# Kernel tuning notes

Hardware: AMD Instinct MI355X
Metric: run time of the kernel (lower is better)

The kernel has to match this reference:

```python
import jax, jax.numpy as jnp
import numpy as np

N = 50000
E = 800000
DIN = 128
# SAGEConv layer dims: (in, out). conv0: input->embed; hidden: 128->64->128->256->512
DIMS = [(128, 128), (128, 64), (64, 128), (128, 256), (256, 512)]
NUM_CLASSES = 4


def setup_inputs() -> dict:
    key = jax.random.key(0)
    ks = jax.random.split(key, 3 * len(DIMS) + 4)
    inp = {"x": jax.random.normal(ks[0], (N, DIN), dtype=jnp.float32)}
    for i, (din, dout) in enumerate(DIMS):
        s = 1.0 / np.sqrt(din).astype(np.float32)
        inp[f"Wl{i}"] = jax.random.normal(ks[1 + 3 * i], (dout, din), dtype=jnp.float32) * s
        inp[f"bl{i}"] = jnp.zeros((dout,), dtype=jnp.float32)
        inp[f"Wr{i}"] = jax.random.normal(ks[2 + 3 * i], (dout, din), dtype=jnp.float32) * s
    dlast = DIMS[-1][1]
    inp["Wout"] = jax.random.normal(ks[-2], (NUM_CLASSES, dlast), dtype=jnp.float32) * (1.0 / np.sqrt(dlast).astype(np.float32))
    inp["bout"] = jnp.zeros((NUM_CLASSES,), dtype=jnp.float32)
    inp["edge_index"] = jax.random.randint(ks[-1], (2, E), 0, N, dtype=jnp.int32)
    return inp


def _forward(x, params, edge_index):
    src, dst = edge_index[0], edge_index[1]
    n = x.shape[0]
    # in-degree (count of incoming edges), clamped to >= 1 as in PyG mean aggregation
    deg = jax.ops.segment_sum(jnp.ones((src.shape[0],), x.dtype), dst, num_segments=n)
    deg_inv = (1.0 / jnp.maximum(deg, 1.0))[:, None]

    def sage(h, Wl, bl, Wr):
        # mean aggregation over incoming neighbors, then lin_l(agg) + lin_r(h)
        agg = jax.ops.segment_sum(h[src], dst, num_segments=n) * deg_inv
        return agg @ Wl.T + bl + h @ Wr.T

    h = x
    for i in range(len(DIMS)):
        h = jax.nn.relu(sage(h, params[f"Wl{i}"], params[f"bl{i}"], params[f"Wr{i}"]))
    logits = h @ params["Wout"].T + params["bout"]
    return jax.nn.softmax(logits, axis=-1)


def reference(x, Wl0, bl0, Wr0, Wl1, bl1, Wr1, Wl2, bl2, Wr2, Wl3, bl3, Wr3,
              Wl4, bl4, Wr4, Wout, bout, edge_index):
    params = {"Wl0": Wl0, "bl0": bl0, "Wr0": Wr0, "Wl1": Wl1, "bl1": bl1, "Wr1": Wr1,
              "Wl2": Wl2, "bl2": bl2, "Wr2": Wr2, "Wl3": Wl3, "bl3": bl3, "Wr3": Wr3,
              "Wl4": Wl4, "bl4": bl4, "Wr4": Wr4, "Wout": Wout, "bout": bout}
    return _forward(x, params, edge_index)
```

## Files before the change

### kernel.cpp

```cpp
#include <hip/hip_runtime.h>
#include <hip/hip_bf16.h>
#include <cstdint>
#include <cstddef>


typedef short bf16x8 __attribute__((ext_vector_type(8)));
typedef float f32x16 __attribute__((ext_vector_type(16)));

static inline int idiv_up(int a, int b) { return (a + b - 1) / b; }

static __device__ __forceinline__ float bf2f(unsigned short u) {
  union { unsigned int i; float f; } v; v.i = ((unsigned int)u) << 16; return v.f;
}
static __device__ __forceinline__ unsigned short f2bf(float f) {
  union { float f; unsigned int i; } v; v.f = f;
  return (unsigned short)((v.i + 0x7FFFu + ((v.i >> 16) & 1u)) >> 16);
}
static __device__ __forceinline__ float lo16(unsigned int u) { return bf2f((unsigned short)(u & 0xffffu)); }
static __device__ __forceinline__ float hi16(unsigned int u) { return bf2f((unsigned short)(u >> 16)); }
static __device__ __forceinline__ unsigned int packbf(float a, float b) {
  return (unsigned int)f2bf(a) | ((unsigned int)f2bf(b) << 16);
}

static __device__ __forceinline__ void gl_lds16(const void* g, void* l) {
  typedef __attribute__((address_space(3))) unsigned int lds_u32;
  typedef __attribute__((address_space(1))) const unsigned int glb_u32;
  __builtin_amdgcn_global_load_lds((glb_u32*)(uintptr_t)g,
                                   (lds_u32*)(unsigned int)(uintptr_t)l, 16, 0, 0);
}

__global__ void k_count_deg(const int* __restrict__ dst, int* __restrict__ deg, int E) {
  const int T = gridDim.x * blockDim.x;
  const int e0 = blockIdx.x * blockDim.x + threadIdx.x;
#pragma unroll
  for (int j = 0; j < 4; ++j) {
    const int e = e0 + j * T;
    if (e < E) atomicAdd(deg + dst[e], 1);
  }
}

__global__ __launch_bounds__(1024)
void k_scan1(const int* __restrict__ deg, int* __restrict__ loc, int* __restrict__ part, int n) {
  __shared__ int wsum[16];
  const int tid = threadIdx.x;
  const int lane = tid & 63, wid = tid >> 6;
  const int i = blockIdx.x * 1024 + tid;
  const int v = (i < n) ? deg[i] : 0;
  int incl = v;
#pragma unroll
  for (int off = 1; off < 64; off <<= 1) {
    int t = __shfl_up(incl, off);
    if (lane >= off) incl += t;
  }
  if (lane == 63) wsum[wid] = incl;
  __syncthreads();
  if (wid == 0) {
    int wv = (lane < 16) ? wsum[lane] : 0;
#pragma unroll
    for (int off = 1; off < 16; off <<= 1) {
      int t = __shfl_up(wv, off);
      if (lane >= off) wv += t;
    }
    if (lane < 16) wsum[lane] = wv;
  }
  __syncthreads();
  const int woff = (wid > 0) ? wsum[wid - 1] : 0;
  if (i < n) loc[i] = woff + incl;
  if (tid == 1023) part[blockIdx.x] = woff + incl;
}

__global__ __launch_bounds__(1024)
void k_scan2(int* __restrict__ part, int nb) {
  __shared__ int wsum[16];
  const int tid = threadIdx.x;
  const int lane = tid & 63, wid = tid >> 6;
  const int v = (tid < nb) ? part[tid] : 0;
  int incl = v;
#pragma unroll
  for (int off = 1; off < 64; off <<= 1) {
    int t = __shfl_up(incl, off);
    if (lane >= off) incl += t;
  }
  if (lane == 63) wsum[wid] = incl;
  __syncthreads();
  if (wid == 0) {
    int wv = (lane < 16) ? wsum[lane] : 0;
#pragma unroll
    for (int off = 1; off < 16; off <<= 1) {
      int t = __shfl_up(wv, off);
      if (lane >= off) wv += t;
    }
    if (lane < 16) wsum[lane] = wv;
  }
  __syncthreads();
  const int woff = (wid > 0) ? wsum[wid - 1] : 0;
  if (tid < nb) part[tid] = woff + incl - v;
  if (tid == 0) part[nb] = wsum[15];
}

__global__ __launch_bounds__(256)
void k_scan3(const int* __restrict__ deg, const int* __restrict__ loc, const int* __restrict__ part,
             int* __restrict__ row_off, int* __restrict__ cursor, float* __restrict__ deg_inv,
             int n, int nb) {
  const int i = blockIdx.x * blockDim.x + threadIdx.x;
  if (i < n) {
    const int v = deg[i];
    const int ro = part[i >> 10] + loc[i] - v;
    row_off[i] = ro;
    cursor[i] = ro;
    deg_inv[i] = 1.0f / (float)((v > 1) ? v : 1);
  }
  if (i == 0) row_off[n] = part[nb];
}

__global__ void k_fill_csr(const int* __restrict__ src, const int* __restrict__ dst,
                           int* __restrict__ cursor, int* __restrict__ esrc, int E) {
  const int T = gridDim.x * blockDim.x;
  const int e0 = blockIdx.x * blockDim.x + threadIdx.x;
  int dv[4], sv[4], pv[4];
#pragma unroll
  for (int j = 0; j < 4; ++j) {
    const int e = e0 + j * T;
    if (e < E) { dv[j] = dst[e]; sv[j] = src[e]; }
  }
#pragma unroll
  for (int j = 0; j < 4; ++j) {
    const int e = e0 + j * T;
    if (e < E) pv[j] = atomicAdd(cursor + dv[j], 1);
  }
#pragma unroll
  for (int j = 0; j < 4; ++j) {
    const int e = e0 + j * T;
    if (e < E) esrc[pv[j]] = sv[j];
  }
}

__global__ __launch_bounds__(256)
void k_conv_x(const float* __restrict__ src, unsigned short* __restrict__ dst, int n4) {
  for (int i = blockIdx.x * blockDim.x + threadIdx.x; i < n4; i += gridDim.x * blockDim.x) {
    const float4 v = *((const float4*)src + i);
    uint2 o;
    o.x = packbf(v.x, v.y);
    o.y = packbf(v.z, v.w);
    *((uint2*)dst + i) = o;
  }
}

struct PackJob { const float* src; unsigned short* dst; int O; int K; int colOff; int Opack; };
struct PackJobs { PackJob j[10]; };

__global__ __launch_bounds__(256)
void k_pack_w(PackJobs jobs) {
  const PackJob J = jobs.j[blockIdx.y];
  const int total = J.O * J.K / 2;
  for (int u = blockIdx.x * blockDim.x + threadIdx.x; u < total; u += gridDim.x * blockDim.x) {
    const int e = u * 2;
    const int col = e / J.K;
    const int k = e - col * J.K;
    const int kt = k >> 6, ch = (k >> 3) & 7, j = k & 7;
    const float f0 = J.src[(size_t)col * J.K + k];
    const float f1 = J.src[(size_t)col * J.K + k + 1];
    const int didx = kt * (J.Opack * 64) + ch * (J.Opack * 8) + (col + J.colOff) * 8 + j;
    ((unsigned int*)J.dst)[didx >> 1] = packbf(f0, f1);
  }
}

static __device__ __forceinline__ void acc_u4(float* acc, const uint4& v) {
  acc[0] += lo16(v.x); acc[1] += hi16(v.x);
  acc[2] += lo16(v.y); acc[3] += hi16(v.y);
  acc[4] += lo16(v.z); acc[5] += hi16(v.z);
  acc[6] += lo16(v.w); acc[7] += hi16(v.w);
}

__global__ __launch_bounds__(256)
void k_agg128(const unsigned short* __restrict__ h, const int* __restrict__ row_off,
              const int* __restrict__ esrc, const float* __restrict__ deg_inv,
              unsigned short* __restrict__ agg, int N) {
  const int node = blockIdx.x * 4 + (threadIdx.x >> 6);
  if (node >= N) return;
  const int lane = threadIdx.x & 63;
  const int g = lane >> 4, c = lane & 15;
  const int s0 = row_off[node], s1 = row_off[node + 1];
  const uint4* hp = (const uint4*)h;
  float acc[8] = {0.f, 0.f, 0.f, 0.f, 0.f, 0.f, 0.f, 0.f};
  for (int i = s0; i < s1; i += 32) {
    int el = i + (lane & 31);
    if (el >= s1) el = s1 - 1;
    const int ev = esrc[el];
    uint4 v[8];
#pragma unroll
    for (int u = 0; u < 8; ++u) {
      if (i + u * 4 < s1) {
        const int e = __shfl(ev, u * 4 + g);
        v[u] = hp[(size_t)e * 16 + c];
      }
    }
#pragma unroll
    for (int u = 0; u < 8; ++u)
      if (i + u * 4 + g < s1) acc_u4(acc, v[u]);
  }
#pragma unroll
  for (int j = 0; j < 8; ++j) {
    acc[j] += __shfl_xor(acc[j], 16);
    acc[j] += __shfl_xor(acc[j], 32);
  }
  if (g == 0) {
    const float di = deg_inv[node];
    uint4 o;
    o.x = packbf(acc[0] * di, acc[1] * di);
    o.y = packbf(acc[2] * di, acc[3] * di);
    o.z = packbf(acc[4] * di, acc[5] * di);
    o.w = packbf(acc[6] * di, acc[7] * di);
    ((uint4*)agg)[(size_t)node * 16 + c] = o;
  }
}

__global__ __launch_bounds__(256)
void k_agg256(const unsigned short* __restrict__ h, const int* __restrict__ row_off,
              const int* __restrict__ esrc, const float* __restrict__ deg_inv,
              unsigned short* __restrict__ agg, int N) {
  const int node = blockIdx.x * 4 + (threadIdx.x >> 6);
  if (node >= N) return;
  const int lane = threadIdx.x & 63;
  const int g = lane >> 5, c = lane & 31;
  const int s0 = row_off[node], s1 = row_off[node + 1];
  const uint4* hp = (const uint4*)h;
  float acc[8] = {0.f, 0.f, 0.f, 0.f, 0.f, 0.f, 0.f, 0.f};
  for (int i = s0; i < s1; i += 32) {
    int el = i + (lane & 31);
    if (el >= s1) el = s1 - 1;
    const int ev = esrc[el];
    uint4 v[16];
#pragma unroll
    for (int u = 0; u < 16; ++u) {
      if (i + u * 2 < s1) {
        const int e = __shfl(ev, u * 2 + g);
        v[u] = hp[(size_t)e * 32 + c];
      }
    }
#pragma unroll
    for (int u = 0; u < 16; ++u)
      if (i + u * 2 + g < s1) acc_u4(acc, v[u]);
  }
#pragma unroll
  for (int j = 0; j < 8; ++j) acc[j] += __shfl_xor(acc[j], 32);
  if (g == 0) {
    const float di = deg_inv[node];
    uint4 o;
    o.x = packbf(acc[0] * di, acc[1] * di);
    o.y = packbf(acc[2] * di, acc[3] * di);
    o.z = packbf(acc[4] * di, acc[5] * di);
    o.w = packbf(acc[6] * di, acc[7] * di);
    ((uint4*)agg)[(size_t)node * 32 + c] = o;
  }
}

__global__ __launch_bounds__(256)
void k_agg64(const unsigned short* __restrict__ h, const int* __restrict__ row_off,
             const int* __restrict__ esrc, const float* __restrict__ deg_inv,
             unsigned short* __restrict__ agg, int N) {
  const int node = blockIdx.x * 4 + (threadIdx.x >> 6);
  if (node >= N) return;
  const int lane = threadIdx.x & 63;
  const int g = lane >> 3, c = lane & 7;
  const int s0 = row_off[node], s1 = row_off[node + 1];
  const uint4* hp = (const uint4*)h;
  float acc[8] = {0.f, 0.f, 0.f, 0.f, 0.f, 0.f, 0.f, 0.f};
  for (int i = s0; i < s1; i += 32) {
    int el = i + (lane & 31);
    if (el >= s1) el = s1 - 1;
    const int ev = esrc[el];
    uint4 v[4];
#pragma unroll
    for (int u = 0; u < 4; ++u) {
      if (i + u * 8 < s1) {
        const int e = __shfl(ev, u * 8 + g);
        v[u] = hp[(size_t)e * 8 + c];
      }
    }
#pragma unroll
    for (int u = 0; u < 4; ++u)
      if (i + u * 8 + g < s1) acc_u4(acc, v[u]);
  }
#pragma unroll
  for (int j = 0; j < 8; ++j) {
    acc[j] += __shfl_xor(acc[j], 8);
    acc[j] += __shfl_xor(acc[j], 16);
    acc[j] += __shfl_xor(acc[j], 32);
  }
  if (g == 0) {
    const float di = deg_inv[node];
    uint4 o;
    o.x = packbf(acc[0] * di, acc[1] * di);
    o.y = packbf(acc[2] * di, acc[3] * di);
    o.z = packbf(acc[4] * di, acc[5] * di);
    o.w = packbf(acc[6] * di, acc[7] * di);
    ((uint4*)agg)[(size_t)node * 8 + c] = o;
  }
}

__global__ __launch_bounds__(256)
void k_agg_post64(const unsigned short* __restrict__ z, const int* __restrict__ row_off,
                  const int* __restrict__ esrc, const float* __restrict__ deg_inv,
                  const float* __restrict__ bias, unsigned short* __restrict__ out, int N) {
  const int node = blockIdx.x * 4 + (threadIdx.x >> 6);
  if (node >= N) return;
  const int lane = threadIdx.x & 63;
  const int g = lane >> 3, c = lane & 7;
  const int s0 = row_off[node], s1 = row_off[node + 1];
  const uint4* zp = (const uint4*)z;
  float acc[8] = {0.f, 0.f, 0.f, 0.f, 0.f, 0.f, 0.f, 0.f};
  for (int i = s0; i < s1; i += 32) {
    int el = i + (lane & 31);
    if (el >= s1) el = s1 - 1;
    const int ev = esrc[el];
    uint4 v[4];
#pragma unroll
    for (int u = 0; u < 4; ++u) {
      if (i + u * 8 < s1) {
        const int e = __shfl(ev, u * 8 + g);
        v[u] = zp[(size_t)e * 16 + c];
      }
    }
#pragma unroll
    for (int u = 0; u < 4; ++u)
      if (i + u * 8 + g < s1) acc_u4(acc, v[u]);
  }
#pragma unroll
  for (int j = 0; j < 8; ++j) {
    acc[j] += __shfl_xor(acc[j], 8);
    acc[j] += __shfl_xor(acc[j], 16);
    acc[j] += __shfl_xor(acc[j], 32);
  }
  if (g == 0) {
    const float di = deg_inv[node];
    const uint4 yr = zp[(size_t)node * 16 + 8 + c];
    float y[8];
    y[0] = lo16(yr.x); y[1] = hi16(yr.x); y[2] = lo16(yr.y); y[3] = hi16(yr.y);
    y[4] = lo16(yr.z); y[5] = hi16(yr.z); y[6] = lo16(yr.w); y[7] = hi16(yr.w);
    float r[8];
#pragma unroll
    for (int j = 0; j < 8; ++j)
      r[j] = fmaxf(acc[j] * di + y[j] + bias[c * 8 + j], 0.f);
    uint4 o;
    o.x = packbf(r[0], r[1]);
    o.y = packbf(r[2], r[3]);
    o.z = packbf(r[4], r[5]);
    o.w = packbf(r[6], r[7]);
    ((uint4*)out)[(size_t)node * 8 + c] = o;
  }
}

template <int WC, int NCB, bool FUSED>
__global__ __launch_bounds__(WC * 128)
void k_sage_gemm(const unsigned short* __restrict__ A0, const unsigned short* __restrict__ B0,
                 const unsigned short* __restrict__ A1, const unsigned short* __restrict__ B1,
                 const float* __restrict__ bias, unsigned short* __restrict__ C,
                 int Nn, int K, int O) {
  constexpr int BN = WC * 64;
  constexpr int T = WC * 128;
  constexpr int ACH = 1024;
  constexpr int LPT = ACH / T;
  __shared__ char lds[2 * 16384];

  const int nrp = (Nn + 127) >> 7;
  const int bid = blockIdx.x;
  const int r8 = bid & 7;
  const int tb = bid >> 3;
  const int cb = tb % NCB;
  const int rowp = (tb / NCB) * 8 + r8;
  if (rowp >= nrp) return;

  const int tid = threadIdx.x;
  const int w = tid >> 6, lane = tid & 63;
  const int wr = w / WC, wc = w % WC;
  const int fr = lane & 31, fq = lane >> 5;
  const int row0 = rowp * 128 + wr * 64;
  const int colb = cb * BN;

  const int KT0 = K >> 6;
  const int NT = FUSED ? 2 * KT0 : KT0;

  f32x16 acc[2][2];
#pragma unroll
  for (int m = 0; m < 2; ++m)
#pragma unroll
    for (int cn = 0; cn < 2; ++cn)
#pragma unroll
      for (int r = 0; r < 16; ++r) acc[m][cn][r] = 0.f;

  auto stage = [&](int buf, int t) {
    const unsigned short* Ab;
    int ktl;
    if (FUSED) {
      const int ph = (t >= KT0) ? 1 : 0;
      Ab = ph ? A1 : A0;
      ktl = t - ph * KT0;
    } else {
      Ab = A0; ktl = t;
    }
    char* lb = lds + buf * 16384;
#pragma unroll
    for (int i = 0; i < LPT; ++i) {
      const int ch = tid + i * T;
      const int ar = ch >> 3, s = ch & 7;
      int g = rowp * 128 + ar;
      if (g >= Nn) g = Nn - 1;
      gl_lds16(Ab + (size_t)g * K + ktl * 64 + ((s ^ (ar & 7)) << 3), lb + ch * 16);
    }
  };

  stage(0, 0);
#pragma unroll 1
  for (int t = 0; t < NT; ++t) {
    asm volatile("s_waitcnt vmcnt(0)" ::: "memory");
    __syncthreads();
    const unsigned short* Bp;
    int ktl;
    if (FUSED) {
      const int ph = (t >= KT0) ? 1 : 0;
      Bp = ph ? B1 : B0;
      ktl = t - ph * KT0;
    } else {
      Bp = B0; ktl = t;
    }
    const unsigned short* Bbase = Bp + (size_t)ktl * (O * 64) + (size_t)(colb + wc * 64) * 8;
    bf16x8 bg[4][2];
#pragma unroll
    for (int k16i = 0; k16i < 4; ++k16i) {
      const int c = k16i * 2 + fq;
#pragma unroll
      for (int cn = 0; cn < 2; ++cn)
        bg[k16i][cn] = *(const bf16x8*)(Bbase + (size_t)c * (O * 8) + (cn * 32 + fr) * 8);
    }
    if (t + 1 < NT) stage((t + 1) & 1, t + 1);
    const char* lb = lds + (t & 1) * 16384;
#pragma unroll
    for (int k16i = 0; k16i < 4; ++k16i) {
      const int c = k16i * 2 + fq;
      bf16x8 af[2];
#pragma unroll
      for (int m = 0; m < 2; ++m) {
        const int rl = wr * 64 + m * 32 + fr;
        af[m] = *(const bf16x8*)(lb + rl * 128 + ((c ^ (rl & 7)) << 4));
      }
#pragma unroll
      for (int m = 0; m < 2; ++m)
#pragma unroll
        for (int cn = 0; cn < 2; ++cn)
          acc[m][cn] = __builtin_amdgcn_mfma_f32_32x32x16_bf16(af[m], bg[k16i][cn], acc[m][cn], 0, 0, 0);
    }
  }

#pragma unroll
  for (int cn = 0; cn < 2; ++cn) {
    const int col = colb + wc * 64 + cn * 32 + fr;
    float bb = 0.f;
    if (FUSED) bb = bias[col];
#pragma unroll
    for (int m = 0; m < 2; ++m) {
#pragma unroll
      for (int reg = 0; reg < 16; ++reg) {
        float v = acc[m][cn][reg];
        if (FUSED) v = fmaxf(v + bb, 0.f);
        const float nb = __shfl_xor(v, 1);
        const int row = row0 + m * 32 + (reg & 3) + 8 * (reg >> 2) + 4 * fq;
        if (!(lane & 1) && row < Nn) {
          *(unsigned int*)(C + (size_t)row * O + col) = packbf(v, nb);
        }
      }
    }
  }
}

__global__ __launch_bounds__(256)
void k_out_softmax(const unsigned short* __restrict__ h, const float* __restrict__ W4,
                   const float* __restrict__ b, float* __restrict__ out, int N) {
  __shared__ float w[2048];
  const int tid = threadIdx.x;
#pragma unroll
  for (int i = 0; i < 8; ++i) w[tid + i * 256] = W4[tid + i * 256];
  __syncthreads();
  const int n = blockIdx.x * 4 + (tid >> 6);
  if (n >= N) return;
  const int lane = tid & 63;
  const unsigned int* hp = (const unsigned int*)h + (size_t)n * 256;
  float a[4] = {0.f, 0.f, 0.f, 0.f};
#pragma unroll
  for (int it = 0; it < 4; ++it) {
    const unsigned int v = hp[it * 64 + lane];
    const float lo = lo16(v);
    const float hi = hi16(v);
    const int k = (it * 64 + lane) * 2;
#pragma unroll
    for (int c = 0; c < 4; ++c)
      a[c] += lo * w[c * 512 + k] + hi * w[c * 512 + k + 1];
  }
#pragma unroll
  for (int off = 32; off > 0; off >>= 1) {
#pragma unroll
    for (int c = 0; c < 4; ++c) a[c] += __shfl_down(a[c], off);
  }
  if (lane == 0) {
    const float l0 = a[0] + b[0], l1 = a[1] + b[1], l2 = a[2] + b[2], l3 = a[3] + b[3];
    const float m = fmaxf(fmaxf(l0, l1), fmaxf(l2, l3));
    const float e0 = expf(l0 - m), e1 = expf(l1 - m), e2 = expf(l2 - m), e3 = expf(l3 - m);
    const float inv = 1.0f / (e0 + e1 + e2 + e3);
    float4 r; r.x = e0 * inv; r.y = e1 * inv; r.z = e2 * inv; r.w = e3 * inv;
    *(float4*)(out + (size_t)n * 4) = r;
  }
}

extern "C" void kernel_launch(void* const* d_in, const int* in_sizes, int n_in,
                              void* d_out, int out_size, void* d_ws, size_t ws_size,
                              hipStream_t stream) {
  const float* x = (const float*)d_in[0];
  const float* Wl[5] = {(const float*)d_in[1], (const float*)d_in[4], (const float*)d_in[7],
                        (const float*)d_in[10], (const float*)d_in[13]};
  const float* bl[5] = {(const float*)d_in[2], (const float*)d_in[5], (const float*)d_in[8],
                        (const float*)d_in[11], (const float*)d_in[14]};
  const float* Wr[5] = {(const float*)d_in[3], (const float*)d_in[6], (const float*)d_in[9],
                        (const float*)d_in[12], (const float*)d_in[15]};
  const float* Wout = (const float*)d_in[16];
  const float* bout = (const float*)d_in[17];
  const int* eidx = (const int*)d_in[18];

  const int N = in_sizes[0] / 128;
  const int E = in_sizes[18] / 2;
  const int* srcI = eidx;
  const int* dstI = eidx + E;

  const int Kd[5] = {128, 128, 64, 128, 256};
  const int Od[5] = {128, 64, 128, 256, 512};

  char* ws = (char*)d_ws;
  size_t p = 0;
  auto alloc = [&](size_t bytes) { size_t r = p; p += (bytes + 255) & ~(size_t)255; return r; };
  int*   deg     = (int*)(ws + alloc((size_t)N * 4));
  int*   row_off = (int*)(ws + alloc((size_t)(N + 1) * 4));
  int*   cursor  = (int*)(ws + alloc((size_t)N * 4));
  float* deg_inv = (float*)(ws + alloc((size_t)N * 4));
  int*   loc     = (int*)(ws + alloc((size_t)N * 4));
  int*   part    = (int*)(ws + alloc((size_t)1032 * 4));
  int*   esrc    = (int*)(ws + alloc((size_t)E * 4));
  unsigned short* xb = (unsigned short*)(ws + alloc((size_t)N * 128 * 2));
  unsigned short* wlb[5];
  unsigned short* wrb[5];
  for (int l = 0; l < 5; ++l) {
    wlb[l] = (unsigned short*)(ws + alloc((size_t)Od[l] * Kd[l] * 2));
    wrb[l] = (unsigned short*)(ws + alloc((size_t)Od[l] * Kd[l] * 2));
  }
  unsigned short* wcat1 = (unsigned short*)(ws + alloc((size_t)128 * 128 * 2));
  unsigned short* bufA = (unsigned short*)(ws + alloc((size_t)N * 512 * 2));
  unsigned short* bufB = (unsigned short*)(ws + alloc((size_t)N * 256 * 2));
  unsigned short* agg  = (unsigned short*)(ws + alloc((size_t)N * 256 * 2));
  (void)ws_size; (void)n_in; (void)out_size;

  k_conv_x<<<128, 256, 0, stream>>>(x, xb, N * 128 / 4);
  PackJobs jobs;
  for (int l = 0; l < 5; ++l) {
    if (l == 1) {
      jobs.j[2] = {Wl[1], wcat1, 64, 128, 0, 128};
      jobs.j[3] = {Wr[1], wcat1, 64, 128, 64, 128};
    } else {
      jobs.j[2 * l]     = {Wl[l], wlb[l], Od[l], Kd[l], 0, Od[l]};
      jobs.j[2 * l + 1] = {Wr[l], wrb[l], Od[l], Kd[l], 0, Od[l]};
    }
  }
  k_pack_w<<<dim3(32, 10), 256, 0, stream>>>(jobs);

  hipMemsetAsync(deg, 0, (size_t)N * 4, stream);
  k_count_deg<<<idiv_up(E, 1024), 256, 0, stream>>>(dstI, deg, E);
  const int nb = idiv_up(N, 1024);
  k_scan1<<<nb, 1024, 0, stream>>>(deg, loc, part, N);
  k_scan2<<<1, 1024, 0, stream>>>(part, nb);
  k_scan3<<<idiv_up(N + 1, 256), 256, 0, stream>>>(deg, loc, part, row_off, cursor, deg_inv, N, nb);
  k_fill_csr<<<idiv_up(E, 1024), 256, 0, stream>>>(srcI, dstI, cursor, esrc, E);

  const int gx8 = 8 * ((idiv_up(N, 128) + 7) / 8);

  k_agg128<<<idiv_up(N, 4), 256, 0, stream>>>(xb, row_off, esrc, deg_inv, agg, N);
  k_sage_gemm<2, 1, true><<<gx8, 256, 0, stream>>>(agg, wlb[0], xb, wrb[0], bl[0], bufA, N, 128, 128);

  k_sage_gemm<2, 1, false><<<gx8, 256, 0, stream>>>(bufA, wcat1, bufA, wcat1, bl[1], agg, N, 128, 128);
  k_agg_post64<<<idiv_up(N, 4), 256, 0, stream>>>(agg, row_off, esrc, deg_inv, bl[1], bufB, N);

  k_agg64<<<idiv_up(N, 4), 256, 0, stream>>>(bufB, row_off, esrc, deg_inv, agg, N);
  k_sage_gemm<2, 1, true><<<gx8, 256, 0, stream>>>(agg, wlb[2], bufB, wrb[2], bl[2], bufA, N, 64, 128);

  k_agg128<<<idiv_up(N, 4), 256, 0, stream>>>(bufA, row_off, esrc, deg_inv, agg, N);
  k_sage_gemm<2, 2, true><<<2 * gx8, 256, 0, stream>>>(agg, wlb[3], bufA, wrb[3], bl[3], bufB, N, 128, 256);

  k_agg256<<<idiv_up(N, 4), 256, 0, stream>>>(bufB, row_off, esrc, deg_inv, agg, N);
  k_sage_gemm<2, 4, true><<<4 * gx8, 256, 0, stream>>>(agg, wlb[4], bufB, wrb[4], bl[4], bufA, N, 256, 512);

  k_out_softmax<<<idiv_up(N, 4), 256, 0, stream>>>(bufA, Wout, bout, (float*)d_out, N);
}
```

Baseline: 393.8 us.

## Fuse output head projection into last SAGE GEMM epilogue and widen CSR build loops

The last SAGE GEMM no longer writes the N×512 bf16 hidden activation to global memory. Each block stages its ReLU'd tile in LDS and computes partial 4-class logits against its 128-column slice of Wout, writing per-column-block partials. A small final kernel sums the four partials, adds the bias and applies softmax. This avoids writing and re-reading about 51 MB of activations, at the cost of an extra LDS pass and two syncs per block. The degree-count and CSR-fill kernels also now process 8 edges per thread with half the grid.

```diff
diff --git a/kernel.cpp b/kernel.cpp
--- a/kernel.cpp
+++ b/kernel.cpp
@@ -33,7 +33,7 @@
   const int T = gridDim.x * blockDim.x;
   const int e0 = blockIdx.x * blockDim.x + threadIdx.x;
 #pragma unroll
-  for (int j = 0; j < 4; ++j) {
+  for (int j = 0; j < 8; ++j) {
     const int e = e0 + j * T;
     if (e < E) atomicAdd(deg + dst[e], 1);
   }
@@ -117,19 +117,19 @@
                            int* __restrict__ cursor, int* __restrict__ esrc, int E) {
   const int T = gridDim.x * blockDim.x;
   const int e0 = blockIdx.x * blockDim.x + threadIdx.x;
-  int dv[4], sv[4], pv[4];
-#pragma unroll
-  for (int j = 0; j < 4; ++j) {
+  int dv[8], sv[8], pv[8];
+#pragma unroll
+  for (int j = 0; j < 8; ++j) {
     const int e = e0 + j * T;
     if (e < E) { dv[j] = dst[e]; sv[j] = src[e]; }
   }
 #pragma unroll
-  for (int j = 0; j < 4; ++j) {
+  for (int j = 0; j < 8; ++j) {
     const int e = e0 + j * T;
     if (e < E) pv[j] = atomicAdd(cursor + dv[j], 1);
   }
 #pragma unroll
-  for (int j = 0; j < 4; ++j) {
+  for (int j = 0; j < 8; ++j) {
     const int e = e0 + j * T;
     if (e < E) esrc[pv[j]] = sv[j];
   }
@@ -351,17 +351,19 @@
   }
 }
 
-template <int WC, int NCB, bool FUSED>
+template <int WC, int NCB, bool FUSED, bool HEAD>
 __global__ __launch_bounds__(WC * 128)
 void k_sage_gemm(const unsigned short* __restrict__ A0, const unsigned short* __restrict__ B0,
                  const unsigned short* __restrict__ A1, const unsigned short* __restrict__ B1,
                  const float* __restrict__ bias, unsigned short* __restrict__ C,
+                 const float* __restrict__ W4g, float* __restrict__ Pb,
                  int Nn, int K, int O) {
   constexpr int BN = WC * 64;
   constexpr int T = WC * 128;
   constexpr int ACH = 1024;
   constexpr int LPT = ACH / T;
-  __shared__ char lds[2 * 16384];
+  constexpr int LDS_SZ = HEAD ? (2 * 16384 + 2048) : (2 * 16384);
+  __shared__ char lds[LDS_SZ];
 
   const int nrp = (Nn + 127) >> 7;
   const int bid = blockIdx.x;
@@ -377,6 +379,21 @@
   const int fr = lane & 31, fq = lane >> 5;
   const int row0 = rowp * 128 + wr * 64;
   const int colb = cb * BN;
+
+  if constexpr (HEAD) {
+    float* w4s = (float*)(lds + 32768);
+#pragma unroll
+    for (int ii = 0; ii < 2 * BN * 4 / T / 2; ++ii) {
+      const int idx = tid * 2 + ii;
+    }
+    const int i0 = tid * 2;
+#pragma unroll
+    for (int ii = 0; ii < 2; ++ii) {
+      const int idx = i0 + ii;
+      if (idx < 4 * BN)
+        w4s[idx] = W4g[(idx >> 7) * 512 + colb + (idx & (BN - 1))];
+    }
+  }
 
   const int KT0 = K >> 6;
   const int NT = FUSED ? 2 * KT0 : KT0;
@@ -452,6 +469,51 @@
     }
   }
 
+  if constexpr (HEAD) {
+    __syncthreads();
+    unsigned int* lh = (unsigned int*)lds;
+    float* w4s = (float*)(lds + 32768);
+#pragma unroll
+    for (int cn = 0; cn < 2; ++cn) {
+      const int coll = wc * 64 + cn * 32 + fr;
+      const float bb = bias[colb + coll];
+#pragma unroll
+      for (int m = 0; m < 2; ++m) {
+#pragma unroll
+        for (int reg = 0; reg < 16; ++reg) {
+          const float v = fmaxf(acc[m][cn][reg] + bb, 0.f);
+          const float nb = __shfl_xor(v, 1);
+          const int rowl = wr * 64 + m * 32 + (reg & 3) + 8 * (reg >> 2) + 4 * fq;
+          if (!(lane & 1)) {
+            const int c2 = coll >> 1;
+            lh[rowl * 64 + ((c2 + rowl) & 63)] = packbf(v, nb);
+          }
+        }
+      }
+    }
+    __syncthreads();
+    if (tid < 128) {
+      const int rowl = tid;
+      float p0 = 0.f, p1 = 0.f, p2 = 0.f, p3 = 0.f;
+#pragma unroll
+      for (int j = 0; j < 64; ++j) {
+        const unsigned int u = lh[rowl * 64 + ((j + rowl) & 63)];
+        const float lo = lo16(u), hi = hi16(u);
+        const int cl = 2 * j, ch = 2 * j + 1;
+        p0 += lo * w4s[cl] + hi * w4s[ch];
+        p1 += lo * w4s[128 + cl] + hi * w4s[128 + ch];
+        p2 += lo * w4s[256 + cl] + hi * w4s[256 + ch];
+        p3 += lo * w4s[384 + cl] + hi * w4s[384 + ch];
+      }
+      const int rg = rowp * 128 + rowl;
+      if (rg < Nn) {
+        float4 o; o.x = p0; o.y = p1; o.z = p2; o.w = p3;
+        *(float4*)(Pb + ((size_t)cb * Nn + rg) * 4) = o;
+      }
+    }
+    return;
+  }
+
 #pragma unroll
   for (int cn = 0; cn < 2; ++cn) {
     const int col = colb + wc * 64 + cn * 32 + fr;
@@ -474,41 +536,23 @@
 }
 
 __global__ __launch_bounds__(256)
-void k_out_softmax(const unsigned short* __restrict__ h, const float* __restrict__ W4,
-                   const float* __restrict__ b, float* __restrict__ out, int N) {
-  __shared__ float w[2048];
-  const int tid = threadIdx.x;
-#pragma unroll
-  for (int i = 0; i < 8; ++i) w[tid + i * 256] = W4[tid + i * 256];
-  __syncthreads();
-  const int n = blockIdx.x * 4 + (tid >> 6);
+void k_head_final(const float* __restrict__ Pb, const float* __restrict__ b,
+                  float* __restrict__ out, int N) {
+  const int n = blockIdx.x * blockDim.x + threadIdx.x;
   if (n >= N) return;
-  const int lane = tid & 63;
-  const unsigned int* hp = (const unsigned int*)h + (size_t)n * 256;
-  float a[4] = {0.f, 0.f, 0.f, 0.f};
-#pragma unroll
-  for (int it = 0; it < 4; ++it) {
-    const unsigned int v = hp[it * 64 + lane];
-    const float lo = lo16(v);
-    const float hi = hi16(v);
-    const int k = (it * 64 + lane) * 2;
-#pragma unroll
-    for (int c = 0; c < 4; ++c)
-      a[c] += lo * w[c * 512 + k] + hi * w[c * 512 + k + 1];
-  }
-#pragma unroll
-  for (int off = 32; off > 0; off >>= 1) {
-#pragma unroll
-    for (int c = 0; c < 4; ++c) a[c] += __shfl_down(a[c], off);
-  }
-  if (lane == 0) {
-    const float l0 = a[0] + b[0], l1 = a[1] + b[1], l2 = a[2] + b[2], l3 = a[3] + b[3];
-    const float m = fmaxf(fmaxf(l0, l1), fmaxf(l2, l3));
-    const float e0 = expf(l0 - m), e1 = expf(l1 - m), e2 = expf(l2 - m), e3 = expf(l3 - m);
-    const float inv = 1.0f / (e0 + e1 + e2 + e3);
-    float4 r; r.x = e0 * inv; r.y = e1 * inv; r.z = e2 * inv; r.w = e3 * inv;
-    *(float4*)(out + (size_t)n * 4) = r;
-  }
+  const float4 q0 = *(const float4*)(Pb + (size_t)n * 4);
+  const float4 q1 = *(const float4*)(Pb + ((size_t)N + n) * 4);
+  const float4 q2 = *(const float4*)(Pb + ((size_t)2 * N + n) * 4);
+  const float4 q3 = *(const float4*)(Pb + ((size_t)3 * N + n) * 4);
+  const float l0 = q0.x + q1.x + q2.x + q3.x + b[0];
+  const float l1 = q0.y + q1.y + q2.y + q3.y + b[1];
+  const float l2 = q0.z + q1.z + q2.z + q3.z + b[2];
+  const float l3 = q0.w + q1.w + q2.w + q3.w + b[3];
+  const float m = fmaxf(fmaxf(l0, l1), fmaxf(l2, l3));
+  const float e0 = expf(l0 - m), e1 = expf(l1 - m), e2 = expf(l2 - m), e3 = expf(l3 - m);
+  const float inv = 1.0f / (e0 + e1 + e2 + e3);
+  float4 r; r.x = e0 * inv; r.y = e1 * inv; r.z = e2 * inv; r.w = e3 * inv;
+  *(float4*)(out + (size_t)n * 4) = r;
 }
 
 extern "C" void kernel_launch(void* const* d_in, const int* in_sizes, int n_in,
@@ -554,6 +598,7 @@
   unsigned short* bufA = (unsigned short*)(ws + alloc((size_t)N * 512 * 2));
   unsigned short* bufB = (unsigned short*)(ws + alloc((size_t)N * 256 * 2));
   unsigned short* agg  = (unsigned short*)(ws + alloc((size_t)N * 256 * 2));
+  float* Pb = (float*)(ws + alloc((size_t)4 * N * 4 * 4));
   (void)ws_size; (void)n_in; (void)out_size;
 
   k_conv_x<<<128, 256, 0, stream>>>(x, xb, N * 128 / 4);
@@ -570,29 +615,34 @@
   k_pack_w<<<dim3(32, 10), 256, 0, stream>>>(jobs);
 
   hipMemsetAsync(deg, 0, (size_t)N * 4, stream);
-  k_count_deg<<<idiv_up(E, 1024), 256, 0, stream>>>(dstI, deg, E);
+  k_count_deg<<<idiv_up(E, 2048), 256, 0, stream>>>(dstI, deg, E);
   const int nb = idiv_up(N, 1024);
   k_scan1<<<nb, 1024, 0, stream>>>(deg, loc, part, N);
   k_scan2<<<1, 1024, 0, stream>>>(part, nb);
   k_scan3<<<idiv_up(N + 1, 256), 256, 0, stream>>>(deg, loc, part, row_off, cursor, deg_inv, N, nb);
-  k_fill_csr<<<idiv_up(E, 1024), 256, 0, stream>>>(srcI, dstI, cursor, esrc, E);
+  k_fill_csr<<<idiv_up(E, 2048), 256, 0, stream>>>(srcI, dstI, cursor, esrc, E);
 
   const int gx8 = 8 * ((idiv_up(N, 128) + 7) / 8);
 
   k_agg128<<<idiv_up(N, 4), 256, 0, stream>>>(xb, row_off, esrc, deg_inv, agg, N);
-  k_sage_gemm<2, 1, true><<<gx8, 256, 0, stream>>>(agg, wlb[0], xb, wrb[0], bl[0], bufA, N, 128, 128);
-
-  k_sage_gemm<2, 1, false><<<gx8, 256, 0, stream>>>(bufA, wcat1, bufA, wcat1, bl[1], agg, N, 128, 128);
+  k_sage_gemm<2, 1, true, false><<<gx8, 256, 0, stream>>>(
+      agg, wlb[0], xb, wrb[0], bl[0], bufA, nullptr, nullptr, N, 128, 128);
+
+  k_sage_gemm<2, 1, false, false><<<gx8, 256, 0, stream>>>(
+      bufA, wcat1, bufA, wcat1, bl[1], agg, nullptr, nullptr, N, 128, 128);
   k_agg_post64<<<idiv_up(N, 4), 256, 0, stream>>>(agg, row_off, esrc, deg_inv, bl[1], bufB, N);
 
   k_agg64<<<idiv_up(N, 4), 256, 0, stream>>>(bufB, row_off, esrc, deg_inv, agg, N);
-  k_sage_gemm<2, 1, true><<<gx8, 256, 0, stream>>>(agg, wlb[2], bufB, wrb[2], bl[2], bufA, N, 64, 128);
+  k_sage_gemm<2, 1, true, false><<<gx8, 256, 0, stream>>>(
+      agg, wlb[2], bufB, wrb[2], bl[2], bufA, nullptr, nullptr, N, 64, 128);
 
   k_agg128<<<idiv_up(N, 4), 256, 0, stream>>>(bufA, row_off, esrc, deg_inv, agg, N);
-  k_sage_gemm<2, 2, true><<<2 * gx8, 256, 0, stream>>>(agg, wlb[3], bufA, wrb[3], bl[3], bufB, N, 128, 256);
+  k_sage_gemm<2, 2, true, false><<<2 * gx8, 256, 0, stream>>>(
+      agg, wlb[3], bufA, wrb[3], bl[3], bufB, nullptr, nullptr, N, 128, 256);
 
   k_agg256<<<idiv_up(N, 4), 256, 0, stream>>>(bufB, row_off, esrc, deg_inv, agg, N);
-  k_sage_gemm<2, 4, true><<<4 * gx8, 256, 0, stream>>>(agg, wlb[4], bufB, wrb[4], bl[4], bufA, N, 256, 512);
-
-  k_out_softmax<<<idiv_up(N, 4), 256, 0, stream>>>(bufA, Wout, bout, (float*)d_out, N);
-}
+  k_sage_gemm<2, 4, true, true><<<4 * gx8, 256, 0, stream>>>(
+      agg, wlb[4], bufB, wrb[4], bl[4], nullptr, Wout, Pb, N, 256, 512);
+
+  k_head_final<<<idiv_up(N, 256), 256, 0, stream>>>(Pb, bout, (float*)d_out, N);
+}
```

After: 449.6 us. 14.2% more time.
